# Optimization experiments

Hardware: AMD Instinct MI355X
Metric: run time of the kernel (lower is better)

## Reference

```python
import jax, jax.numpy as jnp
import numpy as np

TOP_K = 2
EPS = 1e-10


def setup_inputs() -> dict:
    key = jax.random.key(0)
    k1, k2, k3, k4 = jax.random.split(key, 4)
    B, S, H, E = 4, 2048, 1024, 8
    tokens = jax.random.normal(k1, (B, S, H), dtype=jnp.float32)
    router_w = jax.random.normal(k2, (E, H), dtype=jnp.float32) * (1.0 / np.sqrt(H))
    router_b = jax.random.normal(k3, (E,), dtype=jnp.float32) * 0.01
    expert_weights = jax.random.normal(k4, (E, H, H), dtype=jnp.float32) * (1.0 / np.sqrt(H))
    return {"tokens": tokens, "router_w": router_w, "router_b": router_b,
            "expert_weights": expert_weights}


def reference(tokens, router_w, router_b, expert_weights):
    B, S, H = tokens.shape
    E = expert_weights.shape[0]
    # Router (torch Linear: x @ W^T + b)
    logits = jnp.einsum('bsh,eh->bse', tokens, router_w) + router_b  # [B,S,E]
    probs = jax.nn.softmax(logits, axis=-1)
    top_p, top_i = jax.lax.top_k(probs, TOP_K)            # [B,S,K]
    w = top_p / (jnp.sum(top_p, axis=-1, keepdims=True) + EPS)  # normalized weights

    x = tokens.reshape(-1, H)                              # [N,H]
    idx = top_i.reshape(-1, TOP_K)                         # [N,K]
    wf = w.reshape(-1, TOP_K)                              # [N,K]

    # Expert GEMM: compute all experts then gather selected (dense, vectorized
    # equivalent of the sort/pad/grouped-GEMM dispatch; padded rows with
    # original_indices==-1 never contribute to the output).
    y_all = jnp.einsum('nh,ehd->ned', x, expert_weights)   # [N,E,H]
    y_k = jnp.take_along_axis(y_all, idx[:, :, None], axis=1)  # [N,K,H]

    out = jnp.einsum('nk,nkh->nh', wf, y_k)                # weighted combine
    acc = jnp.clip(jnp.sum(wf, axis=-1), EPS, None)        # weight accumulator
    out = (out / acc[:, None]).reshape(B, S, H)

    # epsilon scale tying output to normalized router probs (gradient path)
    scale = 1.0 + jnp.sum(w, axis=-1, keepdims=True) * EPS  # [B,S,1]
    return out * scale
```

## Files before the change

kernel.cpp:

```cpp
#include <hip/hip_runtime.h>
#include <stdint.h>

#define N_TOK 8192
#define H_DIM 1024
#define N_EXP 8
#define MAX_TILES 136

typedef __bf16 bf16x8 __attribute__((ext_vector_type(8)));
typedef float floatx4 __attribute__((ext_vector_type(4)));

typedef __attribute__((address_space(1))) void GV;
typedef __attribute__((address_space(3))) void LV;

static __device__ __forceinline__ unsigned short f2b(float f) {
    union { float f; unsigned int i; } v; v.f = f;
    unsigned int u = v.i;
    return (unsigned short)((u + 0x7FFFu + ((u >> 16) & 1u)) >> 16);
}
static __device__ __forceinline__ float b2f(unsigned short u) {
    union { unsigned int i; float f; } v; v.i = ((unsigned int)u) << 16; return v.f;
}

__global__ __launch_bounds__(256) void k_front(
    const float* __restrict__ tokens,
    const float* __restrict__ router_w,
    const float* __restrict__ router_b,
    const float* __restrict__ W,
    int* __restrict__ sel, float* __restrict__ w_arr,
    unsigned short* __restrict__ tokb,
    unsigned short* __restrict__ Bp)
{
    const int t = threadIdx.x;

    if (blockIdx.x >= 2048) {
        const int idx = blockIdx.x - 2048;
        const int kg = idx & 127;
        const int e  = idx >> 7;
        const int d  = t * 4;
        const float* src = W + ((size_t)e * H_DIM + kg * 8) * H_DIM + d;
        float col[8][4];
#pragma unroll
        for (int j = 0; j < 8; ++j) {
            float4 v = *(const float4*)(src + (size_t)j * H_DIM);
            col[j][0] = v.x; col[j][1] = v.y; col[j][2] = v.z; col[j][3] = v.w;
        }
        unsigned short* dst = Bp + ((size_t)(e * 128 + kg) * H_DIM + d) * 8;
#pragma unroll
        for (int k = 0; k < 4; ++k) {
            unsigned short v[8];
#pragma unroll
            for (int j = 0; j < 8; ++j) v[j] = f2b(col[j][k]);
            *(uint4*)(dst + (size_t)k * 8) = *(uint4*)v;
        }
        return;
    }

    const int wave = t >> 6;
    const int lane = t & 63;
    const int n = blockIdx.x * 4 + wave;

    const float* xp = tokens + (size_t)n * H_DIM + lane * 16;
    float x[16];
#pragma unroll
    for (int i = 0; i < 4; ++i) {
        float4 v = *(const float4*)(xp + i * 4);
        x[i * 4 + 0] = v.x; x[i * 4 + 1] = v.y; x[i * 4 + 2] = v.z; x[i * 4 + 3] = v.w;
    }

    {
        unsigned short xb[16];
#pragma unroll
        for (int j = 0; j < 16; ++j) xb[j] = f2b(x[j]);
        unsigned short* dp = tokb + (size_t)n * H_DIM + lane * 16;
        *(uint4*)(dp)     = *(uint4*)(xb);
        *(uint4*)(dp + 8) = *(uint4*)(xb + 8);
    }

    float acc[N_EXP];
#pragma unroll
    for (int e = 0; e < N_EXP; ++e) {
        const float* wp = router_w + e * H_DIM + lane * 16;
        float s = 0.f;
#pragma unroll
        for (int i = 0; i < 4; ++i) {
            float4 v = *(const float4*)(wp + i * 4);
            s += x[i * 4 + 0] * v.x + x[i * 4 + 1] * v.y
               + x[i * 4 + 2] * v.z + x[i * 4 + 3] * v.w;
        }
        acc[e] = s;
    }

#pragma unroll
    for (int e = 0; e < N_EXP; ++e) {
        float a = acc[e];
#pragma unroll
        for (int off = 32; off > 0; off >>= 1) a += __shfl_xor(a, off);
        acc[e] = a;
    }

    if (lane == 0) {
        float lg[N_EXP];
#pragma unroll
        for (int e = 0; e < N_EXP; ++e) lg[e] = acc[e] + router_b[e];
        int e0 = 0;
#pragma unroll
        for (int e = 1; e < N_EXP; ++e) if (lg[e] > lg[e0]) e0 = e;
        int e1 = -1;
#pragma unroll
        for (int e = 0; e < N_EXP; ++e) {
            if (e == e0) continue;
            if (e1 < 0 || lg[e] > lg[e1]) e1 = e;
        }
        float w0 = 1.f / (1.f + __expf(lg[e1] - lg[e0]));
        float w1 = 1.f - w0;
        sel[n] = e0 | (e1 << 4);
        w_arr[n * 2] = w0;
        w_arr[n * 2 + 1] = w1;
    }
}

__global__ __launch_bounds__(256) void k_scan(
    const int* __restrict__ sel, int* __restrict__ cnt, int* __restrict__ bucket)
{
    __shared__ int ssel[N_TOK + N_TOK / 32];
    __shared__ int sc[256];
    const int e = blockIdx.x;
    const int t = threadIdx.x;
#pragma unroll
    for (int i = 0; i < 32; ++i) {
        int n = i * 256 + t;
        ssel[n + (n >> 5)] = sel[n];
    }
    __syncthreads();
    const int base = t * 32;
    int c = 0;
#pragma unroll
    for (int i = 0; i < 32; ++i) {
        int n = base + i;
        int s = ssel[n + (n >> 5)];
        c += ((s & 15) == e) + (((s >> 4) & 15) == e);
    }
    sc[t] = c;
    __syncthreads();
    for (int off = 1; off < 256; off <<= 1) {
        int v = (t >= off) ? sc[t - off] : 0;
        __syncthreads();
        sc[t] += v;
        __syncthreads();
    }
    int pos = sc[t] - c;
    if (t == 255) cnt[e] = sc[255];
#pragma unroll
    for (int i = 0; i < 32; ++i) {
        int n = base + i;
        int s = ssel[n + (n >> 5)];
        if ((s & 15) == e)        bucket[e * N_TOK + pos++] = 2 * n;
        if (((s >> 4) & 15) == e) bucket[e * N_TOK + pos++] = 2 * n + 1;
    }
}

__global__ __launch_bounds__(256, 4) void k_gemm(
    const unsigned short* __restrict__ tokb,
    const unsigned short* __restrict__ Bp,
    const int* __restrict__ cnt, const int* __restrict__ bucket,
    unsigned short* __restrict__ Y)
{
    const int nt = blockIdx.x & 7;
    const int tile = blockIdx.x >> 3;
    int base = 0, e = 0, mt = -1;
#pragma unroll
    for (int ee = 0; ee < 8; ++ee) {
        int te = (cnt[ee] + 127) >> 7;
        if (tile >= base && tile < base + te) { e = ee; mt = tile - base; }
        base += te;
    }
    if (mt < 0) return;
    const int cnt_local = cnt[e] - mt * 128;

    __shared__ __align__(16) unsigned short Asm[128 * 64];
    __shared__ __align__(16) unsigned short Bsm[8 * 128 * 8];
    __shared__ int rows[128];

    const int t = threadIdx.x;
    if (t < 128)
        rows[t] = (t < cnt_local) ? bucket[e * N_TOK + mt * 128 + t] : -1;
    __syncthreads();

    const int wv = t >> 6, lane = t & 63;
    const int d0 = nt * 128;

    const int p_sw = (lane & 7) ^ ((lane >> 3) & 7);
    const unsigned short* aptr[4];
#pragma unroll
    for (int i = 0; i < 4; ++i) {
        int r = i * 32 + wv * 8 + (lane >> 3);
        int rid = rows[r];
        int tok = (rid >= 0) ? (rid >> 1) : 0;
        aptr[i] = tokb + (size_t)tok * H_DIM + p_sw * 8;
    }
    const unsigned short* bbase = Bp
        + ((size_t)(e * 128 + (t >> 7)) * H_DIM + d0 + (t & 127)) * 8;

    const int w_row = wv >> 1, w_col = wv & 1;
    const int m_lane = lane & 15, quad = lane >> 4;
    const int r7 = m_lane & 7;

    floatx4 acc[4][4];
#pragma unroll
    for (int i = 0; i < 4; ++i)
#pragma unroll
        for (int j = 0; j < 4; ++j) acc[i][j] = (floatx4){0.f, 0.f, 0.f, 0.f};

    for (int kt = 0; kt < H_DIM / 64; ++kt) {
#pragma unroll
        for (int i = 0; i < 4; ++i) {
            __builtin_amdgcn_global_load_lds(
                (GV*)(aptr[i] + kt * 64),
                (LV*)(&Asm[i * 2048 + wv * 512]), 16, 0, 0);
            __builtin_amdgcn_global_load_lds(
                (GV*)(bbase + (size_t)i * 16384 + (size_t)kt * 65536),
                (LV*)(&Bsm[i * 2048 + wv * 512]), 16, 0, 0);
        }
        __syncthreads();

#pragma unroll
        for (int s = 0; s < 2; ++s) {
            bf16x8 a[4], b[4];
#pragma unroll
            for (int i = 0; i < 4; ++i) {
                int row = w_row * 64 + i * 16 + m_lane;
                a[i] = *(const bf16x8*)&Asm[row * 64 + ((s * 4 + quad) ^ r7) * 8];
            }
#pragma unroll
            for (int j = 0; j < 4; ++j)
                b[j] = *(const bf16x8*)&Bsm[((s * 4 + quad) * 128 + w_col * 64 + j * 16 + m_lane) * 8];
#pragma unroll
            for (int i = 0; i < 4; ++i)
#pragma unroll
                for (int j = 0; j < 4; ++j)
                    acc[i][j] = __builtin_amdgcn_mfma_f32_16x16x32_bf16(a[i], b[j], acc[i][j], 0, 0, 0);
        }
        __syncthreads();
    }

#pragma unroll
    for (int i = 0; i < 4; ++i) {
        const int lr_base = w_row * 64 + i * 16 + quad * 4;
#pragma unroll
        for (int reg = 0; reg < 4; ++reg) {
            const int lr = lr_base + reg;
            const int rid = rows[lr];
            if (rid >= 0) {
                unsigned short v[4];
#pragma unroll
                for (int j = 0; j < 4; ++j) v[j] = f2b(acc[i][j][reg]);
                *(uint2*)(Y + (size_t)rid * H_DIM + d0 + w_col * 64 + m_lane * 4) = *(uint2*)v;
            }
        }
    }
}

__global__ __launch_bounds__(256) void k_combine(
    const unsigned short* __restrict__ Y, const float* __restrict__ w_arr,
    float* __restrict__ out)
{
    const int g = blockIdx.x * 256 + threadIdx.x;
    const int n = g >> 7;
    const int c = (g & 127) * 8;
    const unsigned short* y0 = Y + (size_t)(2 * n) * H_DIM + c;
    const unsigned short* y1 = y0 + H_DIM;
    uint4 a = *(const uint4*)y0;
    uint4 b = *(const uint4*)y1;
    const unsigned short* pa = (const unsigned short*)&a;
    const unsigned short* pb = (const unsigned short*)&b;
    const float w0 = w_arr[2 * n], w1 = w_arr[2 * n + 1];
    const int seg = c >> 7;
    const int sl0 = c & 127;
    float* op = out + (size_t)n * H_DIM + seg * 128;
#pragma unroll
    for (int k = 0; k < 8; ++k) {
        int sl = sl0 + k;
        int wc = sl >> 6, m = (sl >> 2) & 15, j = sl & 3;
        int d = wc * 64 + j * 16 + m;
        op[d] = w0 * b2f(pa[k]) + w1 * b2f(pb[k]);
    }
}

extern "C" void kernel_launch(void* const* d_in, const int* in_sizes, int n_in,
                              void* d_out, int out_size, void* d_ws, size_t ws_size,
                              hipStream_t stream)
{
    const float* tokens   = (const float*)d_in[0];
    const float* router_w = (const float*)d_in[1];
    const float* router_b = (const float*)d_in[2];
    const float* W        = (const float*)d_in[3];
    float* out = (float*)d_out;

    char* ws = (char*)d_ws;
    int*   cnt    = (int*)(ws);
    int*   sel    = (int*)(ws + 1024);
    float* w_arr  = (float*)(ws + 34816);
    int*   bucket = (int*)(ws + 100352);
    unsigned short* tokb = (unsigned short*)(ws + 362496);
    unsigned short* Bp   = (unsigned short*)(ws + 17139712);
    unsigned short* Y    = (unsigned short*)(ws + 33916928);

    k_front  <<<2048 + 1024, 256, 0, stream>>>(tokens, router_w, router_b, W,
                                               sel, w_arr, tokb, Bp);
    k_scan   <<<N_EXP, 256, 0, stream>>>(sel, cnt, bucket);
    k_gemm   <<<MAX_TILES * 8, 256, 0, stream>>>(tokb, Bp, cnt, bucket, Y);
    k_combine<<<N_TOK * (H_DIM / 8) / 256, 256, 0, stream>>>(Y, w_arr, out);
}
```

Measured before the change: 193.9 us.

## Double-buffer GEMM LDS tiles and stage combine through shared memory

The expert GEMM now keeps two LDS buffers for the A and B tiles. It prefetches the next K-slice with global_load_lds while the MFMA work runs on the current slice, and uses one waitcnt plus barrier per iteration instead of two syncthreads. The occupancy hint drops from 4 to 2 blocks per CU because LDS use doubles. Separately, the combine kernel loads the permuted bf16 rows into LDS first, so each thread can unscramble its own columns and write contiguous float4 outputs instead of scattered scalar stores.

```diff
diff --git a/kernel.cpp b/kernel.cpp
--- a/kernel.cpp
+++ b/kernel.cpp
@@ -159,7 +159,7 @@
     }
 }
 
-__global__ __launch_bounds__(256, 4) void k_gemm(
+__global__ __launch_bounds__(256, 2) void k_gemm(
     const unsigned short* __restrict__ tokb,
     const unsigned short* __restrict__ Bp,
     const int* __restrict__ cnt, const int* __restrict__ bucket,
@@ -177,8 +177,8 @@
     if (mt < 0) return;
     const int cnt_local = cnt[e] - mt * 128;
 
-    __shared__ __align__(16) unsigned short Asm[128 * 64];
-    __shared__ __align__(16) unsigned short Bsm[8 * 128 * 8];
+    __shared__ __align__(16) unsigned short Asm[2][128 * 64];
+    __shared__ __align__(16) unsigned short Bsm[2][8 * 128 * 8];
     __shared__ int rows[128];
 
     const int t = threadIdx.x;
@@ -211,17 +211,30 @@
 #pragma unroll
         for (int j = 0; j < 4; ++j) acc[i][j] = (floatx4){0.f, 0.f, 0.f, 0.f};
 
+#pragma unroll
+    for (int i = 0; i < 4; ++i) {
+        __builtin_amdgcn_global_load_lds(
+            (GV*)(aptr[i]), (LV*)(&Asm[0][i * 2048 + wv * 512]), 16, 0, 0);
+        __builtin_amdgcn_global_load_lds(
+            (GV*)(bbase + (size_t)i * 16384), (LV*)(&Bsm[0][i * 2048 + wv * 512]), 16, 0, 0);
+    }
+    asm volatile("s_waitcnt vmcnt(0)" ::: "memory");
+    __builtin_amdgcn_s_barrier();
+    asm volatile("" ::: "memory");
+
     for (int kt = 0; kt < H_DIM / 64; ++kt) {
-#pragma unroll
-        for (int i = 0; i < 4; ++i) {
-            __builtin_amdgcn_global_load_lds(
-                (GV*)(aptr[i] + kt * 64),
-                (LV*)(&Asm[i * 2048 + wv * 512]), 16, 0, 0);
-            __builtin_amdgcn_global_load_lds(
-                (GV*)(bbase + (size_t)i * 16384 + (size_t)kt * 65536),
-                (LV*)(&Bsm[i * 2048 + wv * 512]), 16, 0, 0);
-        }
-        __syncthreads();
+        const int cb = kt & 1;
+        if (kt < H_DIM / 64 - 1) {
+#pragma unroll
+            for (int i = 0; i < 4; ++i) {
+                __builtin_amdgcn_global_load_lds(
+                    (GV*)(aptr[i] + (kt + 1) * 64),
+                    (LV*)(&Asm[cb ^ 1][i * 2048 + wv * 512]), 16, 0, 0);
+                __builtin_amdgcn_global_load_lds(
+                    (GV*)(bbase + (size_t)i * 16384 + (size_t)(kt + 1) * 65536),
+                    (LV*)(&Bsm[cb ^ 1][i * 2048 + wv * 512]), 16, 0, 0);
+            }
+        }
 
 #pragma unroll
         for (int s = 0; s < 2; ++s) {
@@ -229,18 +242,21 @@
 #pragma unroll
             for (int i = 0; i < 4; ++i) {
                 int row = w_row * 64 + i * 16 + m_lane;
-                a[i] = *(const bf16x8*)&Asm[row * 64 + ((s * 4 + quad) ^ r7) * 8];
+                a[i] = *(const bf16x8*)&Asm[cb][row * 64 + ((s * 4 + quad) ^ r7) * 8];
             }
 #pragma unroll
             for (int j = 0; j < 4; ++j)
-                b[j] = *(const bf16x8*)&Bsm[((s * 4 + quad) * 128 + w_col * 64 + j * 16 + m_lane) * 8];
+                b[j] = *(const bf16x8*)&Bsm[cb][((s * 4 + quad) * 128 + w_col * 64 + j * 16 + m_lane) * 8];
 #pragma unroll
             for (int i = 0; i < 4; ++i)
 #pragma unroll
                 for (int j = 0; j < 4; ++j)
                     acc[i][j] = __builtin_amdgcn_mfma_f32_16x16x32_bf16(a[i], b[j], acc[i][j], 0, 0, 0);
         }
-        __syncthreads();
+
+        asm volatile("s_waitcnt vmcnt(0)" ::: "memory");
+        __builtin_amdgcn_s_barrier();
+        asm volatile("" ::: "memory");
     }
 
 #pragma unroll
@@ -264,26 +280,39 @@
     const unsigned short* __restrict__ Y, const float* __restrict__ w_arr,
     float* __restrict__ out)
 {
-    const int g = blockIdx.x * 256 + threadIdx.x;
-    const int n = g >> 7;
-    const int c = (g & 127) * 8;
-    const unsigned short* y0 = Y + (size_t)(2 * n) * H_DIM + c;
-    const unsigned short* y1 = y0 + H_DIM;
-    uint4 a = *(const uint4*)y0;
-    uint4 b = *(const uint4*)y1;
-    const unsigned short* pa = (const unsigned short*)&a;
-    const unsigned short* pb = (const unsigned short*)&b;
+    __shared__ __align__(16) unsigned short Ys[4 * H_DIM];
+    const int t = threadIdx.x;
+    const int b = blockIdx.x;
+    const int wv = t >> 6, lane = t & 63;
+    const unsigned short* src = Y + (size_t)b * 4 * H_DIM;
+#pragma unroll
+    for (int r = 0; r < 2; ++r) {
+        __builtin_amdgcn_global_load_lds(
+            (GV*)(src + (size_t)r * 2048 + wv * 512 + lane * 8),
+            (LV*)(&Ys[r * 2048 + wv * 512]), 16, 0, 0);
+    }
+    __syncthreads();
+
+    const int tok = t >> 7;
+    const int n = 2 * b + tok;
+    const int d0 = (t & 127) * 8;
+    const int seg = d0 >> 7;
+    const int dseg = d0 & 127;
+    const int wc = dseg >> 6;
+    const int j  = (dseg >> 4) & 3;
+    const int m0 = dseg & 15;
+    const int sbase = tok * 2 * H_DIM + seg * 128 + wc * 64 + j;
     const float w0 = w_arr[2 * n], w1 = w_arr[2 * n + 1];
-    const int seg = c >> 7;
-    const int sl0 = c & 127;
-    float* op = out + (size_t)n * H_DIM + seg * 128;
+
+    float o[8];
 #pragma unroll
     for (int k = 0; k < 8; ++k) {
-        int sl = sl0 + k;
-        int wc = sl >> 6, m = (sl >> 2) & 15, j = sl & 3;
-        int d = wc * 64 + j * 16 + m;
-        op[d] = w0 * b2f(pa[k]) + w1 * b2f(pb[k]);
-    }
+        int s = sbase + (m0 + k) * 4;
+        o[k] = w0 * b2f(Ys[s]) + w1 * b2f(Ys[s + H_DIM]);
+    }
+    float4* op = (float4*)(out + (size_t)n * H_DIM + d0);
+    op[0] = make_float4(o[0], o[1], o[2], o[3]);
+    op[1] = make_float4(o[4], o[5], o[6], o[7]);
 }
 
 extern "C" void kernel_launch(void* const* d_in, const int* in_sizes, int n_in,
```

Measured after the change: 218.1 us. 12.5% more time.
